# Kernel tuning notes

Measured on AMD Instinct MI355X. Metric: run time of the kernel, lower is better.

Reference implementation:

```python
import jax, jax.numpy as jnp
import numpy as np

B, T, P, N, D, H = 4, 8, 32, 64, 256, 8
M = 4 * D  # mlp hidden
EPS_LN = 1e-5


def _layernorm(x, g, b):
    mu = jnp.mean(x, axis=-1, keepdims=True)
    var = jnp.mean(jnp.square(x - mu), axis=-1, keepdims=True)
    return (x - mu) * jax.lax.rsqrt(var + EPS_LN) * g + b


def _attention(y, qkv_w, qkv_b, proj_w, proj_b, bias=None):
    # y: [Bb, Nn, D]; bias broadcastable to [Bb, H, Nn, Nn]
    Bb, Nn, Dd = y.shape
    hd = Dd // H
    qkv = (y @ qkv_w + qkv_b).reshape(Bb, Nn, 3, H, hd)
    qkv = jnp.transpose(qkv, (2, 0, 3, 1, 4))  # [3, Bb, H, Nn, hd]
    q, k, v = qkv[0], qkv[1], qkv[2]
    s = jnp.einsum('bhnd,bhmd->bhnm', q, k) * (hd ** -0.5)
    if bias is not None:
        s = s + bias
    a = jax.nn.softmax(s, axis=-1)
    o = jnp.einsum('bhnm,bhmd->bhnd', a, v)
    o = jnp.transpose(o, (0, 2, 1, 3)).reshape(Bb, Nn, Dd)
    return o @ proj_w + proj_b


def _mlp(y, fc1_w, fc1_b, fc2_w, fc2_b):
    h = jax.nn.gelu(y @ fc1_w + fc1_b, approximate=False)
    return h @ fc2_w + fc2_b


def setup_inputs():
    key = jax.random.key(0)
    ks = jax.random.split(key, 12)
    lin = lambda k, i, o: (jax.random.normal(k, (i, o), jnp.float32) * (i ** -0.5))
    inp = {}
    inp['x'] = jax.random.normal(ks[0], (B, T, P * N, D), jnp.float32)
    inp['mask'] = jax.random.bernoulli(ks[1], 0.8, (P, N)).astype(jnp.float32)
    inp['patch_adj'] = jax.random.uniform(ks[2], (N, N), jnp.float32, minval=0.01, maxval=1.0)
    inp['dn1_g'] = jnp.ones((D,)); inp['dn1_b'] = jnp.zeros((D,))
    inp['dn2_g'] = jnp.ones((D,)); inp['dn2_b'] = jnp.zeros((D,))
    inp['bn1_g'] = jnp.ones((D,)); inp['bn1_b'] = jnp.zeros((D,))
    inp['d_qkv_w'] = lin(ks[3], D, 3 * D); inp['d_qkv_b'] = jnp.zeros((3 * D,))
    inp['d_proj_w'] = lin(ks[4], D, D); inp['d_proj_b'] = jnp.zeros((D,))
    inp['d_fc1_w'] = lin(ks[5], D, M); inp['d_fc1_b'] = jnp.zeros((M,))
    inp['d_fc2_w'] = lin(ks[6], M, D); inp['d_fc2_b'] = jnp.zeros((D,))
    inp['b_qkv_w'] = lin(ks[7], D, 3 * D); inp['b_qkv_b'] = jnp.zeros((3 * D,))
    inp['b_proj_w'] = lin(ks[8], D, D); inp['b_proj_b'] = jnp.zeros((D,))
    inp['b_fc1_w'] = lin(ks[9], D, M); inp['b_fc1_b'] = jnp.zeros((M,))
    inp['b_fc2_w'] = lin(ks[10], M, D); inp['b_fc2_b'] = jnp.zeros((D,))
    return inp


def reference(x, mask, patch_adj, dn1_g, dn1_b, dn2_g, dn2_b, bn1_g, bn1_b,
              d_qkv_w, d_qkv_b, d_proj_w, d_proj_b, d_fc1_w, d_fc1_b, d_fc2_w, d_fc2_b,
              b_qkv_w, b_qkv_b, b_proj_w, b_proj_b, b_fc1_w, b_fc1_b, b_fc2_w, b_fc2_b):
    x5 = x.reshape(B, T, P, N, D)
    m = mask[None, None, :, :, None]  # [1,1,P,N,1]
    # --- depth (windowed) attention with log-adjacency bias ---
    y = _layernorm(x5, dn1_g, dn1_b).reshape(B * T * P, N, D)
    bias = jnp.log(patch_adj + 1e-6)[None, None, :, :]  # [1,1,N,N]
    y = _attention(y, d_qkv_w, d_qkv_b, d_proj_w, d_proj_b, bias=bias)
    x5 = x5 + y.reshape(B, T, P, N, D) * m
    # --- depth MLP ---
    y = _mlp(_layernorm(x5, dn2_g, dn2_b), d_fc1_w, d_fc1_b, d_fc2_w, d_fc2_b)
    x5 = x5 + y * m
    # --- masked mean-pool over nodes, breadth attention over patches ---
    z = (x5 * m).sum(axis=3) / jnp.clip(m.sum(axis=3), 1.0, None)  # [B,T,P,D]
    z = _layernorm(z.reshape(B * T, P, D), bn1_g, bn1_b)
    z = _attention(z, b_qkv_w, b_qkv_b, b_proj_w, b_proj_b)
    z = _mlp(z, b_fc1_w, b_fc1_b, b_fc2_w, b_fc2_b)
    x5 = x5 + z.reshape(B, T, P, D)[:, :, :, None, :]
    return x5.reshape(B, T, P * N, D)
```

## Files before the change

kernel.cpp:

```cpp
#include <hip/hip_runtime.h>
#include <hip/hip_bf16.h>
#include <math.h>

typedef __attribute__((ext_vector_type(8))) short short8;
typedef __attribute__((ext_vector_type(4))) float floatx4;

__device__ __forceinline__ unsigned short f2u(float f) {
    union { float f; unsigned int i; } c; c.f = f;
    unsigned int r = c.i + 0x7FFF + ((c.i >> 16) & 1);
    return (unsigned short)(r >> 16);
}
__device__ __forceinline__ float gelu_exact(float x) {
    return 0.5f * x * (1.0f + erff(x * 0.7071067811865475f));
}

__global__ __launch_bounds__(256) void pack_weights_k(
    const float* __restrict__ W1, const float* __restrict__ W2,
    const float* __restrict__ Wqkv, const float* __restrict__ Wp,
    const float* __restrict__ bW1, const float* __restrict__ bW2,
    const float* __restrict__ bWqkv, const float* __restrict__ bWp,
    const float* __restrict__ adj,
    unsigned short* __restrict__ W1t, unsigned short* __restrict__ W2t,
    unsigned short* __restrict__ Wqkvt, unsigned short* __restrict__ Wpt,
    unsigned short* __restrict__ bW1t, unsigned short* __restrict__ bW2t,
    unsigned short* __restrict__ bWqkvt, unsigned short* __restrict__ bWpt,
    float* __restrict__ Ladj)
{
    int b = blockIdx.x, t = threadIdx.x;
    if (b < 1024) {
        W1t[(size_t)b * 256 + t] = f2u(W1[(size_t)t * 1024 + b]);
    } else if (b < 1280) {
        int n = b - 1024;
        for (int it = 0; it < 4; ++it) {
            int k = it * 256 + t;
            W2t[(size_t)n * 1024 + k] = f2u(W2[(size_t)k * 256 + n]);
        }
    } else if (b < 2048) {
        int c = b - 1280;
        Wqkvt[(size_t)c * 256 + t] = f2u(Wqkv[(size_t)t * 768 + c]);
    } else if (b < 2304) {
        int c = b - 2048;
        Wpt[(size_t)c * 256 + t] = f2u(Wp[(size_t)t * 256 + c]);
    } else if (b < 3328) {
        int c = b - 2304;
        bW1t[(size_t)c * 256 + t] = f2u(bW1[(size_t)t * 1024 + c]);
    } else if (b < 3584) {
        int n = b - 3328;
        for (int it = 0; it < 4; ++it) {
            int k = it * 256 + t;
            bW2t[(size_t)n * 1024 + k] = f2u(bW2[(size_t)k * 256 + n]);
        }
    } else if (b < 4352) {
        int c = b - 3584;
        bWqkvt[(size_t)c * 256 + t] = f2u(bWqkv[(size_t)t * 768 + c]);
    } else if (b < 4608) {
        int c = b - 4352;
        bWpt[(size_t)c * 256 + t] = f2u(bWp[(size_t)t * 256 + c]);
    } else {
        for (int i = 0; i < 16; ++i) {
            int idx = t * 16 + i;
            Ladj[idx] = logf(adj[idx] + 1e-6f);
        }
    }
}

__global__ __launch_bounds__(256, 2) void attn_mfma_k(
    const float* __restrict__ x, const float* __restrict__ mask,
    const float* __restrict__ Ladj,
    const float* __restrict__ g1, const float* __restrict__ be1,
    const unsigned short* __restrict__ Wqkvt, const float* __restrict__ Bqkv,
    const unsigned short* __restrict__ Wpt, const float* __restrict__ Bp,
    float* __restrict__ out)
{
    __shared__ __align__(16) unsigned char smem[33792];
    unsigned short (*Ybuf)[264] = (unsigned short (*)[264])smem;
    unsigned short (*qb)[40]    = (unsigned short (*)[40])(smem);
    unsigned short (*kb)[40]    = (unsigned short (*)[40])(smem + 5120);
    unsigned short (*Vt)[72]    = (unsigned short (*)[72])(smem + 10240);
    unsigned short (*Pb)[72]    = (unsigned short (*)[72])(smem + 14848);
    unsigned short (*Ob)[40]    = (unsigned short (*)[40])(smem + 24064);

    int w = blockIdx.x, p = w & 31, t = threadIdx.x;
    int wave = t >> 6, lane = t & 63;
    int l15 = lane & 15, kw = lane >> 4;
    size_t base = (size_t)w * 16384;

    for (int it = 0; it < 16; ++it) {
        int r = it * 4 + wave;
        float vals[4]; float sum = 0.f, sq = 0.f;
#pragma unroll
        for (int k2 = 0; k2 < 4; ++k2) {
            float vv = x[base + (size_t)r * 256 + lane + 64 * k2];
            vals[k2] = vv; sum += vv; sq += vv * vv;
        }
        for (int o = 32; o > 0; o >>= 1) { sum += __shfl_xor(sum, o); sq += __shfl_xor(sq, o); }
        float mu = sum * (1.f / 256.f);
        float var = sq * (1.f / 256.f) - mu * mu;
        float rstd = rsqrtf(var + 1e-5f);
#pragma unroll
        for (int k2 = 0; k2 < 4; ++k2) {
            int c = lane + 64 * k2;
            Ybuf[r][c] = f2u((vals[k2] - mu) * rstd * g1[c] + be1[c]);
            out[base + (size_t)r * 256 + c] = vals[k2];
        }
    }
    __syncthreads();

    short8 ay[8];
#pragma unroll
    for (int ks = 0; ks < 8; ++ks)
        ay[ks] = *(const short8*)(&Ybuf[wave * 16 + l15][ks * 32 + kw * 8]);

    floatx4 oacc[16];
#pragma unroll
    for (int cf = 0; cf < 16; ++cf) {
        float bb = Bp[cf * 16 + l15];
        oacc[cf] = (floatx4){bb, bb, bb, bb};
    }
    __syncthreads();

    const float sc = 0.17677669529663689f;

    for (int h = 0; h < 8; ++h) {
        floatx4 qacc[6];
#pragma unroll
        for (int cf = 0; cf < 6; ++cf) {
            int gcol = (cf >> 1) * 256 + h * 32 + (cf & 1) * 16 + l15;
            float bb = Bqkv[gcol];
            qacc[cf] = (floatx4){bb, bb, bb, bb};
        }
#pragma unroll
        for (int ks = 0; ks < 8; ++ks) {
            short8 bw[6];
#pragma unroll
            for (int cf = 0; cf < 6; ++cf) {
                int gcol = (cf >> 1) * 256 + h * 32 + (cf & 1) * 16 + l15;
                bw[cf] = *(const short8*)(Wqkvt + (size_t)gcol * 256 + ks * 32 + kw * 8);
            }
#pragma unroll
            for (int cf = 0; cf < 6; ++cf)
                qacc[cf] = __builtin_amdgcn_mfma_f32_16x16x32_bf16(ay[ks], bw[cf], qacc[cf], 0, 0, 0);
        }
#pragma unroll
        for (int cf = 0; cf < 6; ++cf)
#pragma unroll
            for (int jj = 0; jj < 4; ++jj) {
                int r = wave * 16 + kw * 4 + jj;
                int d = (cf & 1) * 16 + l15;
                unsigned short ub = f2u(qacc[cf][jj]);
                if (cf < 2) qb[r][d] = ub;
                else if (cf < 4) kb[r][d] = ub;
                else Vt[d][r] = ub;
            }
        __syncthreads();

        short8 aq = *(const short8*)(&qb[wave * 16 + l15][kw * 8]);
        floatx4 sacc[4];
#pragma unroll
        for (int cf = 0; cf < 4; ++cf) {
            short8 bk = *(const short8*)(&kb[cf * 16 + l15][kw * 8]);
            sacc[cf] = __builtin_amdgcn_mfma_f32_16x16x32_bf16(aq, bk,
                        (floatx4){0.f, 0.f, 0.f, 0.f}, 0, 0, 0);
        }
#pragma unroll
        for (int jj = 0; jj < 4; ++jj) {
            int r = wave * 16 + kw * 4 + jj;
            float s0 = sacc[0][jj] * sc + Ladj[r * 64 + 0 * 16 + l15];
            float s1 = sacc[1][jj] * sc + Ladj[r * 64 + 1 * 16 + l15];
            float s2 = sacc[2][jj] * sc + Ladj[r * 64 + 2 * 16 + l15];
            float s3 = sacc[3][jj] * sc + Ladj[r * 64 + 3 * 16 + l15];
            float mx = fmaxf(fmaxf(s0, s1), fmaxf(s2, s3));
            mx = fmaxf(mx, __shfl_xor(mx, 1));
            mx = fmaxf(mx, __shfl_xor(mx, 2));
            mx = fmaxf(mx, __shfl_xor(mx, 4));
            mx = fmaxf(mx, __shfl_xor(mx, 8));
            float e0 = __expf(s0 - mx), e1 = __expf(s1 - mx);
            float e2 = __expf(s2 - mx), e3 = __expf(s3 - mx);
            float sum = e0 + e1 + e2 + e3;
            sum += __shfl_xor(sum, 1);
            sum += __shfl_xor(sum, 2);
            sum += __shfl_xor(sum, 4);
            sum += __shfl_xor(sum, 8);
            float inv = 1.f / sum;
            Pb[r][0 * 16 + l15] = f2u(e0 * inv);
            Pb[r][1 * 16 + l15] = f2u(e1 * inv);
            Pb[r][2 * 16 + l15] = f2u(e2 * inv);
            Pb[r][3 * 16 + l15] = f2u(e3 * inv);
        }

        floatx4 oacc2[2];
#pragma unroll
        for (int cf2 = 0; cf2 < 2; ++cf2) oacc2[cf2] = (floatx4){0.f, 0.f, 0.f, 0.f};
#pragma unroll
        for (int ks = 0; ks < 2; ++ks) {
            short8 ap = *(const short8*)(&Pb[wave * 16 + l15][ks * 32 + kw * 8]);
#pragma unroll
            for (int cf2 = 0; cf2 < 2; ++cf2) {
                short8 bv = *(const short8*)(&Vt[cf2 * 16 + l15][ks * 32 + kw * 8]);
                oacc2[cf2] = __builtin_amdgcn_mfma_f32_16x16x32_bf16(ap, bv, oacc2[cf2], 0, 0, 0);
            }
        }
#pragma unroll
        for (int cf2 = 0; cf2 < 2; ++cf2)
#pragma unroll
            for (int jj = 0; jj < 4; ++jj)
                Ob[wave * 16 + kw * 4 + jj][cf2 * 16 + l15] = f2u(oacc2[cf2][jj]);
        __syncthreads();

        short8 ao = *(const short8*)(&Ob[wave * 16 + l15][kw * 8]);
#pragma unroll
        for (int cf = 0; cf < 16; ++cf) {
            short8 bw = *(const short8*)(Wpt + (size_t)(cf * 16 + l15) * 256 + h * 32 + kw * 8);
            oacc[cf] = __builtin_amdgcn_mfma_f32_16x16x32_bf16(ao, bw, oacc[cf], 0, 0, 0);
        }
    }

#pragma unroll
    for (int jj = 0; jj < 4; ++jj) {
        int r = wave * 16 + kw * 4 + jj;
        float mv = mask[p * 64 + r];
#pragma unroll
        for (int cf = 0; cf < 16; ++cf) {
            size_t idx = base + (size_t)r * 256 + cf * 16 + l15;
            out[idx] += oacc[cf][jj] * mv;
        }
    }
}

__global__ __launch_bounds__(256, 2) void mlp_mfma_k(
    const float* __restrict__ mask,
    const float* __restrict__ g2, const float* __restrict__ be2,
    const unsigned short* __restrict__ W1t, const float* __restrict__ B1,
    const unsigned short* __restrict__ W2t, const float* __restrict__ B2,
    float* __restrict__ out, float* __restrict__ zsum)
{
    __shared__ __align__(16) unsigned char smem[33792];
    unsigned short (*Ybuf)[264] = (unsigned short (*)[264])smem;
    unsigned short (*Hbuf)[72]  = (unsigned short (*)[72])smem;
    unsigned short* Wbuf        = (unsigned short*)(smem + 9216);

    int w = blockIdx.x, p = w & 31, t = threadIdx.x;
    int wave = t >> 6, lane = t & 63;
    int l15 = lane & 15, kw = lane >> 4;
    size_t base = (size_t)w * 16384;

    for (int it = 0; it < 16; ++it) {
        int r = it * 4 + wave;
        float vals[4]; float sum = 0.f, sq = 0.f;
#pragma unroll
        for (int k2 = 0; k2 < 4; ++k2) {
            float vv = out[base + (size_t)r * 256 + lane + 64 * k2];
            vals[k2] = vv; sum += vv; sq += vv * vv;
        }
        for (int o = 32; o > 0; o >>= 1) { sum += __shfl_xor(sum, o); sq += __shfl_xor(sq, o); }
        float mu = sum * (1.f / 256.f);
        float var = sq * (1.f / 256.f) - mu * mu;
        float rstd = rsqrtf(var + 1e-5f);
#pragma unroll
        for (int k2 = 0; k2 < 4; ++k2) {
            int c = lane + 64 * k2;
            Ybuf[r][c] = f2u((vals[k2] - mu) * rstd * g2[c] + be2[c]);
        }
    }
    __syncthreads();

    short8 ay[8];
#pragma unroll
    for (int ks = 0; ks < 8; ++ks)
        ay[ks] = *(const short8*)(&Ybuf[wave * 16 + l15][ks * 32 + kw * 8]);
    __syncthreads();

    floatx4 oacc[4][4];
#pragma unroll
    for (int m = 0; m < 4; ++m)
#pragma unroll
        for (int j = 0; j < 4; ++j) {
            float bb = B2[wave * 64 + j * 16 + l15];
            oacc[m][j] = (floatx4){bb, bb, bb, bb};
        }

    for (int pass = 0; pass < 16; ++pass) {
        floatx4 facc[4];
#pragma unroll
        for (int j = 0; j < 4; ++j) {
            float bb = B1[pass * 64 + j * 16 + l15];
            facc[j] = (floatx4){bb, bb, bb, bb};
        }
        {
            int nr = t >> 2, c = t & 3;
            *(short8*)(Wbuf + nr * 40 + c * 8) =
                *(const short8*)(W1t + (size_t)(pass * 64 + nr) * 256 + c * 8);
        }
        __syncthreads();
        for (int ks = 0; ks < 8; ++ks) {
            if (ks + 1 < 8) {
                int nr = t >> 2, c = t & 3;
                *(short8*)(Wbuf + ((ks + 1) & 1) * 2560 + nr * 40 + c * 8) =
                    *(const short8*)(W1t + (size_t)(pass * 64 + nr) * 256 + (ks + 1) * 32 + c * 8);
            }
            int hh = (ks & 1) * 2560;
            short8 bf[4];
#pragma unroll
            for (int j = 0; j < 4; ++j)
                bf[j] = *(const short8*)(Wbuf + hh + (j * 16 + l15) * 40 + kw * 8);
#pragma unroll
            for (int j = 0; j < 4; ++j)
                facc[j] = __builtin_amdgcn_mfma_f32_16x16x32_bf16(ay[ks], bf[j], facc[j], 0, 0, 0);
            __syncthreads();
        }
#pragma unroll
        for (int j = 0; j < 4; ++j)
#pragma unroll
            for (int jj = 0; jj < 4; ++jj)
                Hbuf[wave * 16 + kw * 4 + jj][j * 16 + l15] = f2u(gelu_exact(facc[j][jj]));
        __syncthreads();

        for (int ks2 = 0; ks2 < 2; ++ks2) {
            for (int it = 0; it < 4; ++it) {
                int idx = it * 256 + t;
                int nr = idx >> 2, c = idx & 3;
                *(short8*)(Wbuf + nr * 40 + c * 8) =
                    *(const short8*)(W2t + (size_t)nr * 1024 + pass * 64 + ks2 * 32 + c * 8);
            }
            __syncthreads();
            short8 af[4], bf[4];
#pragma unroll
            for (int m = 0; m < 4; ++m)
                af[m] = *(const short8*)(&Hbuf[m * 16 + l15][ks2 * 32 + kw * 8]);
#pragma unroll
            for (int j = 0; j < 4; ++j)
                bf[j] = *(const short8*)(Wbuf + (wave * 64 + j * 16 + l15) * 40 + kw * 8);
#pragma unroll
            for (int m = 0; m < 4; ++m)
#pragma unroll
                for (int j = 0; j < 4; ++j)
                    oacc[m][j] = __builtin_amdgcn_mfma_f32_16x16x32_bf16(af[m], bf[j], oacc[m][j], 0, 0, 0);
            __syncthreads();
        }
    }

    float zp[4] = {0.f, 0.f, 0.f, 0.f};
#pragma unroll
    for (int m = 0; m < 4; ++m) {
#pragma unroll
        for (int jj = 0; jj < 4; ++jj) {
            int r = m * 16 + kw * 4 + jj;
            float mv = mask[p * 64 + r];
#pragma unroll
            for (int j = 0; j < 4; ++j) {
                size_t idx = base + (size_t)r * 256 + wave * 64 + j * 16 + l15;
                float nv = out[idx] + oacc[m][j][jj] * mv;
                out[idx] = nv;
                zp[j] += mv * nv;
            }
        }
    }
#pragma unroll
    for (int j = 0; j < 4; ++j) {
        zp[j] += __shfl_xor(zp[j], 16);
        zp[j] += __shfl_xor(zp[j], 32);
    }
    if (kw == 0) {
#pragma unroll
        for (int j = 0; j < 4; ++j)
            zsum[(size_t)w * 256 + wave * 64 + j * 16 + l15] = zp[j];
    }
}

__global__ __launch_bounds__(256) void zcompute_k(
    const float* __restrict__ zsum, const float* __restrict__ mask,
    const float* __restrict__ gvec, const float* __restrict__ bvec,
    const unsigned short* __restrict__ bWqkvt, const float* __restrict__ Bqkv,
    const unsigned short* __restrict__ bWpt, const float* __restrict__ Bp,
    const unsigned short* __restrict__ bW1t, const float* __restrict__ B1,
    const unsigned short* __restrict__ bW2t, const float* __restrict__ B2,
    float* __restrict__ zout)
{
    __shared__ unsigned short Zbuf[32][264];
    __shared__ unsigned short Z2[32][264];
    __shared__ unsigned short qb[32][40], kb[32][40], Vt[32][40], Pb[32][40], Ob[32][40];
    __shared__ unsigned short Hbuf[32][72];
    __shared__ float msh[32];
    int bt = blockIdx.x, t = threadIdx.x;
    int wave = t >> 6, lane = t & 63;
    int l15 = lane & 15, kw = lane >> 4;
    int rt = wave & 1, cq = wave >> 1;

    if (t < 32) {
        float s = 0.f;
        for (int nn = 0; nn < 64; ++nn) s += mask[t * 64 + nn];
        msh[t] = fmaxf(s, 1.f);
    }
    __syncthreads();

    for (int it = 0; it < 8; ++it) {
        int r = it * 4 + wave;
        float inv_m = 1.f / msh[r];
        float vals[4]; float sum = 0.f, sq = 0.f;
#pragma unroll
        for (int k2 = 0; k2 < 4; ++k2) {
            float vv = zsum[(size_t)bt * 8192 + (size_t)r * 256 + lane + 64 * k2] * inv_m;
            vals[k2] = vv; sum += vv; sq += vv * vv;
        }
        for (int o = 32; o > 0; o >>= 1) { sum += __shfl_xor(sum, o); sq += __shfl_xor(sq, o); }
        float mu = sum * (1.f / 256.f);
        float var = sq * (1.f / 256.f) - mu * mu;
        float rstd = rsqrtf(var + 1e-5f);
#pragma unroll
        for (int k2 = 0; k2 < 4; ++k2) {
            int c = lane + 64 * k2;
            Zbuf[r][c] = f2u((vals[k2] - mu) * rstd * gvec[c] + bvec[c]);
        }
    }
    __syncthreads();

    short8 ay[8];
#pragma unroll
    for (int ks = 0; ks < 8; ++ks)
        ay[ks] = *(const short8*)(&Zbuf[rt * 16 + l15][ks * 32 + kw * 8]);

    floatx4 pacc[8];
#pragma unroll
    for (int cf = 0; cf < 8; ++cf) {
        float bb = Bp[cq * 128 + cf * 16 + l15];
        pacc[cf] = (floatx4){bb, bb, bb, bb};
    }
    const float sc = 0.17677669529663689f;

    for (int h = 0; h < 8; ++h) {
        floatx4 qacc[3];
#pragma unroll
        for (int cf = 0; cf < 3; ++cf) {
            int c96 = cq * 48 + cf * 16 + l15;
            int gcol = (c96 >> 5) * 256 + h * 32 + (c96 & 31);
            float bb = Bqkv[gcol];
            qacc[cf] = (floatx4){bb, bb, bb, bb};
        }
#pragma unroll
        for (int ks = 0; ks < 8; ++ks) {
#pragma unroll
            for (int cf = 0; cf < 3; ++cf) {
                int c96 = cq * 48 + cf * 16 + l15;
                int gcol = (c96 >> 5) * 256 + h * 32 + (c96 & 31);
                short8 bw = *(const short8*)(bWqkvt + (size_t)gcol * 256 + ks * 32 + kw * 8);
                qacc[cf] = __builtin_amdgcn_mfma_f32_16x16x32_bf16(ay[ks], bw, qacc[cf], 0, 0, 0);
            }
        }
#pragma unroll
        for (int cf = 0; cf < 3; ++cf) {
            int c96 = cq * 48 + cf * 16 + l15;
            int which = c96 >> 5, d = c96 & 31;
#pragma unroll
            for (int jj = 0; jj < 4; ++jj) {
                int r = rt * 16 + kw * 4 + jj;
                unsigned short ub = f2u(qacc[cf][jj]);
                if (which == 0) qb[r][d] = ub;
                else if (which == 1) kb[r][d] = ub;
                else Vt[d][r] = ub;
            }
        }
        __syncthreads();
        if (wave < 2) {
            short8 aq = *(const short8*)(&qb[wave * 16 + l15][kw * 8]);
            floatx4 sacc[2];
#pragma unroll
            for (int cf = 0; cf < 2; ++cf) {
                short8 bk = *(const short8*)(&kb[cf * 16 + l15][kw * 8]);
                sacc[cf] = __builtin_amdgcn_mfma_f32_16x16x32_bf16(aq, bk,
                            (floatx4){0.f, 0.f, 0.f, 0.f}, 0, 0, 0);
            }
#pragma unroll
            for (int jj = 0; jj < 4; ++jj) {
                float s0 = sacc[0][jj] * sc;
                float s1 = sacc[1][jj] * sc;
                float mx = fmaxf(s0, s1);
                mx = fmaxf(mx, __shfl_xor(mx, 1));
                mx = fmaxf(mx, __shfl_xor(mx, 2));
                mx = fmaxf(mx, __shfl_xor(mx, 4));
                mx = fmaxf(mx, __shfl_xor(mx, 8));
                float e0 = __expf(s0 - mx), e1 = __expf(s1 - mx);
                float sum = e0 + e1;
                sum += __shfl_xor(sum, 1);
                sum += __shfl_xor(sum, 2);
                sum += __shfl_xor(sum, 4);
                sum += __shfl_xor(sum, 8);
                float inv = 1.f / sum;
                int r = wave * 16 + kw * 4 + jj;
                Pb[r][l15] = f2u(e0 * inv);
                Pb[r][16 + l15] = f2u(e1 * inv);
            }
        }
        __syncthreads();
        {
            short8 ap = *(const short8*)(&Pb[rt * 16 + l15][kw * 8]);
            short8 bv = *(const short8*)(&Vt[cq * 16 + l15][kw * 8]);
            floatx4 oo = __builtin_amdgcn_mfma_f32_16x16x32_bf16(ap, bv,
                          (floatx4){0.f, 0.f, 0.f, 0.f}, 0, 0, 0);
#pragma unroll
            for (int jj = 0; jj < 4; ++jj)
                Ob[rt * 16 + kw * 4 + jj][cq * 16 + l15] = f2u(oo[jj]);
        }
        __syncthreads();
        {
            short8 ao = *(const short8*)(&Ob[rt * 16 + l15][kw * 8]);
#pragma unroll
            for (int cf = 0; cf < 8; ++cf) {
                int gcol = cq * 128 + cf * 16 + l15;
                short8 bw = *(const short8*)(bWpt + (size_t)gcol * 256 + h * 32 + kw * 8);
                pacc[cf] = __builtin_amdgcn_mfma_f32_16x16x32_bf16(ao, bw, pacc[cf], 0, 0, 0);
            }
        }
        __syncthreads();
    }
#pragma unroll
    for (int cf = 0; cf < 8; ++cf)
#pragma unroll
        for (int jj = 0; jj < 4; ++jj)
            Z2[rt * 16 + kw * 4 + jj][cq * 128 + cf * 16 + l15] = f2u(pacc[cf][jj]);
    __syncthreads();

    short8 az[8];
#pragma unroll
    for (int ks = 0; ks < 8; ++ks)
        az[ks] = *(const short8*)(&Z2[rt * 16 + l15][ks * 32 + kw * 8]);

    floatx4 oacc2[8];
#pragma unroll
    for (int cf = 0; cf < 8; ++cf) {
        float bb = B2[cq * 128 + cf * 16 + l15];
        oacc2[cf] = (floatx4){bb, bb, bb, bb};
    }
    for (int pass = 0; pass < 16; ++pass) {
        floatx4 facc[2];
#pragma unroll
        for (int cf = 0; cf < 2; ++cf) {
            int col = pass * 64 + cq * 32 + cf * 16 + l15;
            float bb = B1[col];
            facc[cf] = (floatx4){bb, bb, bb, bb};
        }
#pragma unroll
        for (int ks = 0; ks < 8; ++ks) {
#pragma unroll
            for (int cf = 0; cf < 2; ++cf) {
                int col = pass * 64 + cq * 32 + cf * 16 + l15;
                short8 bw = *(const short8*)(bW1t + (size_t)col * 256 + ks * 32 + kw * 8);
                facc[cf] = __builtin_amdgcn_mfma_f32_16x16x32_bf16(az[ks], bw, facc[cf], 0, 0, 0);
            }
        }
#pragma unroll
        for (int cf = 0; cf < 2; ++cf)
#pragma unroll
            for (int jj = 0; jj < 4; ++jj)
                Hbuf[rt * 16 + kw * 4 + jj][cq * 32 + cf * 16 + l15] = f2u(gelu_exact(facc[cf][jj]));
        __syncthreads();
#pragma unroll
        for (int ks = 0; ks < 2; ++ks) {
            short8 ah = *(const short8*)(&Hbuf[rt * 16 + l15][ks * 32 + kw * 8]);
#pragma unroll
            for (int cf = 0; cf < 8; ++cf) {
                int gcol = cq * 128 + cf * 16 + l15;
                short8 bw = *(const short8*)(bW2t + (size_t)gcol * 1024 + pass * 64 + ks * 32 + kw * 8);
                oacc2[cf] = __builtin_amdgcn_mfma_f32_16x16x32_bf16(ah, bw, oacc2[cf], 0, 0, 0);
            }
        }
        __syncthreads();
    }
#pragma unroll
    for (int cf = 0; cf < 8; ++cf)
#pragma unroll
        for (int jj = 0; jj < 4; ++jj) {
            int r = rt * 16 + kw * 4 + jj;
            int c = cq * 128 + cf * 16 + l15;
            zout[(size_t)bt * 8192 + r * 256 + c] = oacc2[cf][jj];
        }
}

__global__ __launch_bounds__(256) void zadd_k(
    const float* __restrict__ zout, float* __restrict__ out)
{
    int w = blockIdx.x, t = threadIdx.x;
    size_t base = (size_t)w * 16384;
    float zv = zout[(size_t)w * 256 + t];
    for (int nn = 0; nn < 64; ++nn)
        out[base + (size_t)nn * 256 + t] += zv;
}

extern "C" void kernel_launch(void* const* d_in, const int* in_sizes, int n_in,
                              void* d_out, int out_size, void* d_ws, size_t ws_size,
                              hipStream_t stream) {
    (void)in_sizes; (void)n_in; (void)out_size; (void)ws_size;
    const float* x        = (const float*)d_in[0];
    const float* mask     = (const float*)d_in[1];
    const float* adj      = (const float*)d_in[2];
    const float* dn1_g    = (const float*)d_in[3];
    const float* dn1_b    = (const float*)d_in[4];
    const float* dn2_g    = (const float*)d_in[5];
    const float* dn2_b    = (const float*)d_in[6];
    const float* bn1_g    = (const float*)d_in[7];
    const float* bn1_b    = (const float*)d_in[8];
    const float* d_qkv_w  = (const float*)d_in[9];
    const float* d_qkv_b  = (const float*)d_in[10];
    const float* d_proj_w = (const float*)d_in[11];
    const float* d_proj_b = (const float*)d_in[12];
    const float* d_fc1_w  = (const float*)d_in[13];
    const float* d_fc1_b  = (const float*)d_in[14];
    const float* d_fc2_w  = (const float*)d_in[15];
    const float* d_fc2_b  = (const float*)d_in[16];
    const float* b_qkv_w  = (const float*)d_in[17];
    const float* b_qkv_b  = (const float*)d_in[18];
    const float* b_proj_w = (const float*)d_in[19];
    const float* b_proj_b = (const float*)d_in[20];
    const float* b_fc1_w  = (const float*)d_in[21];
    const float* b_fc1_b  = (const float*)d_in[22];
    const float* b_fc2_w  = (const float*)d_in[23];
    const float* b_fc2_b  = (const float*)d_in[24];
    float* out = (float*)d_out;

    unsigned short* W1t    = (unsigned short*)d_ws;
    unsigned short* W2t    = W1t + 262144;
    unsigned short* Wqkvt  = W2t + 262144;
    unsigned short* Wpt    = Wqkvt + 196608;
    unsigned short* bW1t   = Wpt + 65536;
    unsigned short* bW2t   = bW1t + 262144;
    unsigned short* bWqkvt = bW2t + 262144;
    unsigned short* bWpt   = bWqkvt + 196608;
    float* Ladj            = (float*)(bWpt + 65536);
    float* zsum            = Ladj + 4096;
    float* zout            = zsum + 262144;

    pack_weights_k<<<4609, 256, 0, stream>>>(d_fc1_w, d_fc2_w, d_qkv_w, d_proj_w,
                                             b_fc1_w, b_fc2_w, b_qkv_w, b_proj_w, adj,
                                             W1t, W2t, Wqkvt, Wpt,
                                             bW1t, bW2t, bWqkvt, bWpt, Ladj);
    attn_mfma_k<<<1024, 256, 0, stream>>>(x, mask, Ladj, dn1_g, dn1_b,
                                          Wqkvt, d_qkv_b, Wpt, d_proj_b, out);
    mlp_mfma_k<<<1024, 256, 0, stream>>>(mask, dn2_g, dn2_b,
                                         W1t, d_fc1_b, W2t, d_fc2_b, out, zsum);
    zcompute_k<<<32, 256, 0, stream>>>(zsum, mask, bn1_g, bn1_b,
                                       bWqkvt, b_qkv_b, bWpt, b_proj_b,
                                       bW1t, b_fc1_b, bW2t, b_fc2_b, zout);
    zadd_k<<<1024, 256, 0, stream>>>(zout, out);
}
```

Measured before the change: 827.1 us.

## Fuse depth attention and depth MLP into a single per-window kernel

```diff
diff --git a/kernel.cpp b/kernel.cpp
--- a/kernel.cpp
+++ b/kernel.cpp
@@ -64,13 +64,16 @@
     }
 }
 
-__global__ __launch_bounds__(256, 2) void attn_mfma_k(
+__global__ __launch_bounds__(256, 2) void attn_mlp_k(
     const float* __restrict__ x, const float* __restrict__ mask,
     const float* __restrict__ Ladj,
     const float* __restrict__ g1, const float* __restrict__ be1,
     const unsigned short* __restrict__ Wqkvt, const float* __restrict__ Bqkv,
     const unsigned short* __restrict__ Wpt, const float* __restrict__ Bp,
-    float* __restrict__ out)
+    const float* __restrict__ g2, const float* __restrict__ be2,
+    const unsigned short* __restrict__ W1t, const float* __restrict__ B1,
+    const unsigned short* __restrict__ W2t, const float* __restrict__ B2,
+    float* __restrict__ out, float* __restrict__ zsum)
 {
     __shared__ __align__(16) unsigned char smem[33792];
     unsigned short (*Ybuf)[264] = (unsigned short (*)[264])smem;
@@ -79,6 +82,8 @@
     unsigned short (*Vt)[72]    = (unsigned short (*)[72])(smem + 10240);
     unsigned short (*Pb)[72]    = (unsigned short (*)[72])(smem + 14848);
     unsigned short (*Ob)[40]    = (unsigned short (*)[40])(smem + 24064);
+    unsigned short (*Hbuf)[72]  = (unsigned short (*)[72])smem;
+    unsigned short* Wbuf        = (unsigned short*)(smem + 9216);
 
     int w = blockIdx.x, p = w & 31, t = threadIdx.x;
     int wave = t >> 6, lane = t & 63;
@@ -101,7 +106,6 @@
         for (int k2 = 0; k2 < 4; ++k2) {
             int c = lane + 64 * k2;
             Ybuf[r][c] = f2u((vals[k2] - mu) * rstd * g1[c] + be1[c]);
-            out[base + (size_t)r * 256 + c] = vals[k2];
         }
     }
     __syncthreads();
@@ -219,64 +223,66 @@
     for (int jj = 0; jj < 4; ++jj) {
         int r = wave * 16 + kw * 4 + jj;
         float mv = mask[p * 64 + r];
+        float xv[16];
+#pragma unroll
+        for (int cf = 0; cf < 16; ++cf)
+            xv[cf] = x[base + (size_t)r * 256 + cf * 16 + l15];
+#pragma unroll
+        for (int cf = 0; cf < 16; ++cf)
+            oacc[cf][jj] = xv[cf] + oacc[cf][jj] * mv;
+    }
+
+    float g2r[16], be2r[16];
+#pragma unroll
+    for (int cf = 0; cf < 16; ++cf) {
+        g2r[cf]  = g2[cf * 16 + l15];
+        be2r[cf] = be2[cf * 16 + l15];
+    }
+#pragma unroll
+    for (int jj = 0; jj < 4; ++jj) {
+        int r = wave * 16 + kw * 4 + jj;
+        float s1 = 0.f, s2 = 0.f;
 #pragma unroll
         for (int cf = 0; cf < 16; ++cf) {
-            size_t idx = base + (size_t)r * 256 + cf * 16 + l15;
-            out[idx] += oacc[cf][jj] * mv;
-        }
-    }
-}
-
-__global__ __launch_bounds__(256, 2) void mlp_mfma_k(
-    const float* __restrict__ mask,
-    const float* __restrict__ g2, const float* __restrict__ be2,
-    const unsigned short* __restrict__ W1t, const float* __restrict__ B1,
-    const unsigned short* __restrict__ W2t, const float* __restrict__ B2,
-    float* __restrict__ out, float* __restrict__ zsum)
-{
-    __shared__ __align__(16) unsigned char smem[33792];
-    unsigned short (*Ybuf)[264] = (unsigned short (*)[264])smem;
-    unsigned short (*Hbuf)[72]  = (unsigned short (*)[72])smem;
-    unsigned short* Wbuf        = (unsigned short*)(smem + 9216);
-
-    int w = blockIdx.x, p = w & 31, t = threadIdx.x;
-    int wave = t >> 6, lane = t & 63;
-    int l15 = lane & 15, kw = lane >> 4;
-    size_t base = (size_t)w * 16384;
-
-    for (int it = 0; it < 16; ++it) {
-        int r = it * 4 + wave;
-        float vals[4]; float sum = 0.f, sq = 0.f;
-#pragma unroll
-        for (int k2 = 0; k2 < 4; ++k2) {
-            float vv = out[base + (size_t)r * 256 + lane + 64 * k2];
-            vals[k2] = vv; sum += vv; sq += vv * vv;
-        }
-        for (int o = 32; o > 0; o >>= 1) { sum += __shfl_xor(sum, o); sq += __shfl_xor(sq, o); }
-        float mu = sum * (1.f / 256.f);
-        float var = sq * (1.f / 256.f) - mu * mu;
+            float v = oacc[cf][jj];
+            s1 += v; s2 += v * v;
+        }
+        s1 += __shfl_xor(s1, 1); s2 += __shfl_xor(s2, 1);
+        s1 += __shfl_xor(s1, 2); s2 += __shfl_xor(s2, 2);
+        s1 += __shfl_xor(s1, 4); s2 += __shfl_xor(s2, 4);
+        s1 += __shfl_xor(s1, 8); s2 += __shfl_xor(s2, 8);
+        float mu = s1 * (1.f / 256.f);
+        float var = s2 * (1.f / 256.f) - mu * mu;
         float rstd = rsqrtf(var + 1e-5f);
 #pragma unroll
-        for (int k2 = 0; k2 < 4; ++k2) {
-            int c = lane + 64 * k2;
-            Ybuf[r][c] = f2u((vals[k2] - mu) * rstd * g2[c] + be2[c]);
-        }
+        for (int cf = 0; cf < 16; ++cf)
+            out[base + (size_t)r * 256 + cf * 16 + l15] = oacc[cf][jj];
+#pragma unroll
+        for (int cf = 0; cf < 16; ++cf)
+            oacc[cf][jj] = (oacc[cf][jj] - mu) * rstd * g2r[cf] + be2r[cf];
     }
     __syncthreads();
 
-    short8 ay[8];
+#pragma unroll
+    for (int jj = 0; jj < 4; ++jj) {
+        int r = wave * 16 + kw * 4 + jj;
+#pragma unroll
+        for (int cf = 0; cf < 16; ++cf)
+            Ybuf[r][cf * 16 + l15] = f2u(oacc[cf][jj]);
+    }
+    short8 ay2[8];
 #pragma unroll
     for (int ks = 0; ks < 8; ++ks)
-        ay[ks] = *(const short8*)(&Ybuf[wave * 16 + l15][ks * 32 + kw * 8]);
+        ay2[ks] = *(const short8*)(&Ybuf[wave * 16 + l15][ks * 32 + kw * 8]);
     __syncthreads();
 
-    floatx4 oacc[4][4];
+    floatx4 macc[4][4];
 #pragma unroll
     for (int m = 0; m < 4; ++m)
 #pragma unroll
         for (int j = 0; j < 4; ++j) {
             float bb = B2[wave * 64 + j * 16 + l15];
-            oacc[m][j] = (floatx4){bb, bb, bb, bb};
+            macc[m][j] = (floatx4){bb, bb, bb, bb};
         }
 
     for (int pass = 0; pass < 16; ++pass) {
@@ -305,7 +311,7 @@
                 bf[j] = *(const short8*)(Wbuf + hh + (j * 16 + l15) * 40 + kw * 8);
 #pragma unroll
             for (int j = 0; j < 4; ++j)
-                facc[j] = __builtin_amdgcn_mfma_f32_16x16x32_bf16(ay[ks], bf[j], facc[j], 0, 0, 0);
+                facc[j] = __builtin_amdgcn_mfma_f32_16x16x32_bf16(ay2[ks], bf[j], facc[j], 0, 0, 0);
             __syncthreads();
         }
 #pragma unroll
@@ -334,7 +340,7 @@
             for (int m = 0; m < 4; ++m)
 #pragma unroll
                 for (int j = 0; j < 4; ++j)
-                    oacc[m][j] = __builtin_amdgcn_mfma_f32_16x16x32_bf16(af[m], bf[j], oacc[m][j], 0, 0, 0);
+                    macc[m][j] = __builtin_amdgcn_mfma_f32_16x16x32_bf16(af[m], bf[j], macc[m][j], 0, 0, 0);
             __syncthreads();
         }
     }
@@ -342,16 +348,23 @@
     float zp[4] = {0.f, 0.f, 0.f, 0.f};
 #pragma unroll
     for (int m = 0; m < 4; ++m) {
+        float ov[4][4];
+#pragma unroll
+        for (int jj = 0; jj < 4; ++jj) {
+            int r = m * 16 + kw * 4 + jj;
+#pragma unroll
+            for (int j = 0; j < 4; ++j)
+                ov[jj][j] = out[base + (size_t)r * 256 + wave * 64 + j * 16 + l15];
+        }
 #pragma unroll
         for (int jj = 0; jj < 4; ++jj) {
             int r = m * 16 + kw * 4 + jj;
             float mv = mask[p * 64 + r];
 #pragma unroll
             for (int j = 0; j < 4; ++j) {
-                size_t idx = base + (size_t)r * 256 + wave * 64 + j * 16 + l15;
-                float nv = out[idx] + oacc[m][j][jj] * mv;
-                out[idx] = nv;
-                zp[j] += mv * nv;
+                float nv2 = ov[jj][j] + macc[m][j][jj] * mv;
+                out[base + (size_t)r * 256 + wave * 64 + j * 16 + l15] = nv2;
+                zp[j] += mv * nv2;
             }
         }
     }
@@ -632,10 +645,11 @@
                                              b_fc1_w, b_fc2_w, b_qkv_w, b_proj_w, adj,
                                              W1t, W2t, Wqkvt, Wpt,
                                              bW1t, bW2t, bWqkvt, bWpt, Ladj);
-    attn_mfma_k<<<1024, 256, 0, stream>>>(x, mask, Ladj, dn1_g, dn1_b,
-                                          Wqkvt, d_qkv_b, Wpt, d_proj_b, out);
-    mlp_mfma_k<<<1024, 256, 0, stream>>>(mask, dn2_g, dn2_b,
-                                         W1t, d_fc1_b, W2t, d_fc2_b, out, zsum);
+    attn_mlp_k<<<1024, 256, 0, stream>>>(x, mask, Ladj, dn1_g, dn1_b,
+                                         Wqkvt, d_qkv_b, Wpt, d_proj_b,
+                                         dn2_g, dn2_b,
+                                         W1t, d_fc1_b, W2t, d_fc2_b,
+                                         out, zsum);
     zcompute_k<<<32, 256, 0, stream>>>(zsum, mask, bn1_g, bn1_b,
                                        bWqkvt, b_qkv_b, bWpt, b_proj_b,
                                        bW1t, b_fc1_b, bW2t, b_fc2_b, zout);
```

Result: faster. 790.8 us (-4.4%).
